# Performance work log

Hardware: AMD Instinct MI355X
Metric: run time of the kernel (lower is better)

The kernel has to match this reference:

```python
import jax, jax.numpy as jnp
import numpy as np

B, T, C = 32, 4096, 128  # batch, TRAIN_LEN, channels (= nb_filters)
K, D = 3, 8              # kernel_size, dilation_rate
F = 128                  # nb_filters


def my_deconv1d(x, kernel, bias, dilation):
    """Faithful MyDeConv1D: dilated transposed conv via scatter-add.

    Original: raw[b,t,k,f] = sum_c(x[b,t,c]*W[c,k,f] + bias[f])
              => einsum + C_in*bias (bias added before the C-sum!).
    Then each raw[b,t,j,:] contributes to output position t + j*d,
    summed over t (gather_nd + double reduce_sum), keep last T steps.
    """
    b, t_len, c_in = x.shape
    _, k_size, f_out = kernel.shape
    raw = jnp.einsum('btc,ckf->btkf', x, kernel) + c_in * bias  # (B,T,K,F)
    final_len = t_len + (k_size - 1) * dilation
    pos = (jnp.arange(t_len)[:, None] + jnp.arange(k_size)[None, :] * dilation).reshape(-1)  # (T*K,)
    out = jnp.zeros((b, final_len, f_out), x.dtype)
    out = out.at[:, pos, :].add(raw.reshape(b, t_len * k_size, f_out))
    return out[:, -t_len:, :]


def setup_inputs() -> dict:
    key = jax.random.key(0)
    k1, k2, k3, k4, k5 = jax.random.split(key, 5)
    he = lambda k, shape, fan_in: jax.random.normal(k, shape, jnp.float32) * np.sqrt(2.0 / fan_in)
    return {
        'x': jax.random.normal(k1, (B, T, C), jnp.float32),
        'kernel1': he(k2, (C, K, F), C * K),
        'bias1': jnp.zeros((F,), jnp.float32),
        'kernel2': he(k3, (F, K, F), F * K),
        'bias2': jnp.zeros((F,), jnp.float32),
    }


def reference(x, kernel1, bias1, kernel2, bias2):
    # TemporalDeConvBlock: repeat_times=2, residual=True, norm_way=None,
    # dropout_rate=0 (identity), activation='relu', identity shape-match.
    h = jax.nn.relu(my_deconv1d(x, kernel1, bias1, D))
    h = jax.nn.relu(my_deconv1d(h, kernel2, bias2, D))
    return jax.nn.relu(h + x)
```

## Files before the change

### kernel.cpp

```cpp
#include <hip/hip_runtime.h>
#include <hip/hip_fp16.h>

#define BATCH 32
#define TLEN  4096
#define CH    128
#define KW    3
#define DIL   8

#define BM    128
#define HR    (BM + 2 * DIL)
#define WROWS (BM + 4 * DIL)
#define LDSC  132

typedef _Float16 f16x8 __attribute__((ext_vector_type(8)));
typedef float    f32x4 __attribute__((ext_vector_type(4)));

__global__ void prep_weights_kernel(const float* __restrict__ W1,
                                    const float* __restrict__ W2,
                                    _Float16* __restrict__ Wt1,
                                    _Float16* __restrict__ Wt2) {
    const int total = KW * CH * CH;
    int idx = blockIdx.x * 256 + threadIdx.x;
    if (idx >= 2 * total) return;
    const float* W  = (idx < total) ? W1 : W2;
    _Float16*    Wt = (idx < total) ? Wt1 : Wt2;
    int r = idx % total;
    int j = r / (CH * CH);
    int f = (r / CH) % CH;
    int c = r % CH;
    Wt[j * CH * CH + f * CH + c] = (_Float16)W[c * (KW * CH) + j * CH + f];
}

__global__ __launch_bounds__(256)
void fused_deconv_kernel(const float* __restrict__ x,
                         const _Float16* __restrict__ Wt1,
                         const float* __restrict__ bias1,
                         const _Float16* __restrict__ Wt2,
                         const float* __restrict__ bias2,
                         float* __restrict__ out)
{
    __shared__ __align__(16) _Float16 xs[WROWS][LDSC];
    __shared__ __align__(16) _Float16 hs[HR][LDSC];

    const int tid  = threadIdx.x;
    const int lane = tid & 63;
    const int wid  = tid >> 6;
    const int l15  = lane & 15;
    const int kg   = lane >> 4;
    const int nc   = wid << 5;

    const int bt0 = blockIdx.x;
    const int bt  = (bt0 & 7) * 128 + (bt0 >> 3);

    const int b  = bt >> 5;
    const int t0 = (bt & 31) << 7;

    f16x8 w1[12][2];
#pragma unroll
    for (int ks = 0; ks < 12; ++ks) {
        const int j  = ks >> 2;
        const int c0 = (ks & 3) << 5;
        const _Float16* wb = Wt1 + (size_t)j * (CH * CH) + c0 + kg * 8;
        w1[ks][0] = *(const f16x8*)(wb + (nc + l15) * CH);
        w1[ks][1] = *(const f16x8*)(wb + (nc + 16 + l15) * CH);
    }

#pragma unroll
    for (int p = 0; p < 10; ++p) {
        const int i   = tid + 256 * p;
        const int row = i >> 4;
        const int c8  = (i & 15) << 3;
        const int t   = t0 + row;
        f16x8 o;
        if (t < TLEN) {
            const float* xp = x + ((size_t)b * TLEN + t) * CH + c8;
            f32x4 v0 = *(const f32x4*)(xp + 0);
            f32x4 v1 = *(const f32x4*)(xp + 4);
            o[0] = (_Float16)v0[0]; o[1] = (_Float16)v0[1];
            o[2] = (_Float16)v0[2]; o[3] = (_Float16)v0[3];
            o[4] = (_Float16)v1[0]; o[5] = (_Float16)v1[1];
            o[6] = (_Float16)v1[2]; o[7] = (_Float16)v1[3];
        } else {
            o = (f16x8){};
        }
        *(f16x8*)&xs[row][c8] = o;
    }

    const float bv1_0 = 128.0f * bias1[nc + l15];
    const float bv1_1 = 128.0f * bias1[nc + 16 + l15];
    const float bv2_0 = 128.0f * bias2[nc + l15];
    const float bv2_1 = 128.0f * bias2[nc + 16 + l15];

    __syncthreads();

    f32x4 acc1[9][2];
#pragma unroll
    for (int m = 0; m < 9; ++m) {
        acc1[m][0] = (f32x4){0.f, 0.f, 0.f, 0.f};
        acc1[m][1] = (f32x4){0.f, 0.f, 0.f, 0.f};
    }
#pragma unroll
    for (int ks = 0; ks < 12; ++ks) {
        const int j     = ks >> 2;
        const int c0    = (ks & 3) << 5;
        const int shift = (2 - j) * DIL;
#pragma unroll
        for (int m = 0; m < 9; ++m) {
            f16x8 af = *(const f16x8*)&xs[m * 16 + shift + l15][c0 + kg * 8];
            acc1[m][0] = __builtin_amdgcn_mfma_f32_16x16x32_f16(af, w1[ks][0], acc1[m][0], 0, 0, 0);
            acc1[m][1] = __builtin_amdgcn_mfma_f32_16x16x32_f16(af, w1[ks][1], acc1[m][1], 0, 0, 0);
        }
    }

    f16x8 w2[12][2];
#pragma unroll
    for (int ks = 0; ks < 12; ++ks) {
        const int j  = ks >> 2;
        const int c0 = (ks & 3) << 5;
        const _Float16* wb = Wt2 + (size_t)j * (CH * CH) + c0 + kg * 8;
        w2[ks][0] = *(const f16x8*)(wb + (nc + l15) * CH);
        w2[ks][1] = *(const f16x8*)(wb + (nc + 16 + l15) * CH);
    }

#pragma unroll
    for (int m = 0; m < 9; ++m) {
#pragma unroll
        for (int nn = 0; nn < 2; ++nn) {
            const float bv = nn ? bv1_1 : bv1_0;
            const int f = nc + nn * 16 + l15;
#pragma unroll
            for (int i = 0; i < 4; ++i) {
                const int r = m * 16 + kg * 4 + i;
                const int u = t0 + r;
                const int nv = 1 + (u < TLEN - DIL) + (u < TLEN - 2 * DIL);
                float v = acc1[m][nn][i] + (float)nv * bv;
                v = fmaxf(v, 0.0f);
                hs[r][f] = (u < TLEN) ? (_Float16)v : (_Float16)0.0f;
            }
        }
    }
    __syncthreads();

    f32x4 acc2[8][2];
#pragma unroll
    for (int m = 0; m < 8; ++m) {
        acc2[m][0] = (f32x4){0.f, 0.f, 0.f, 0.f};
        acc2[m][1] = (f32x4){0.f, 0.f, 0.f, 0.f};
    }
#pragma unroll
    for (int ks = 0; ks < 12; ++ks) {
        const int j     = ks >> 2;
        const int c0    = (ks & 3) << 5;
        const int shift = (2 - j) * DIL;
#pragma unroll
        for (int m = 0; m < 8; ++m) {
            f16x8 af = *(const f16x8*)&hs[m * 16 + shift + l15][c0 + kg * 8];
            acc2[m][0] = __builtin_amdgcn_mfma_f32_16x16x32_f16(af, w2[ks][0], acc2[m][0], 0, 0, 0);
            acc2[m][1] = __builtin_amdgcn_mfma_f32_16x16x32_f16(af, w2[ks][1], acc2[m][1], 0, 0, 0);
        }
    }

#pragma unroll
    for (int m = 0; m < 8; ++m) {
#pragma unroll
        for (int nn = 0; nn < 2; ++nn) {
            const float bv = nn ? bv2_1 : bv2_0;
            const int f = nc + nn * 16 + l15;
#pragma unroll
            for (int i = 0; i < 4; ++i) {
                const int r = m * 16 + kg * 4 + i;
                const int t = t0 + r;
                const int nv = 1 + (t < TLEN - DIL) + (t < TLEN - 2 * DIL);
                float v = acc2[m][nn][i] + (float)nv * bv;
                v = fmaxf(v, 0.0f);
                v = fmaxf(v + (float)xs[r][f], 0.0f);
                out[((size_t)b * TLEN + t) * CH + f] = v;
            }
        }
    }
}

extern "C" void kernel_launch(void* const* d_in, const int* in_sizes, int n_in,
                              void* d_out, int out_size, void* d_ws, size_t ws_size,
                              hipStream_t stream) {
    const float* x  = (const float*)d_in[0];
    const float* W1 = (const float*)d_in[1];
    const float* b1 = (const float*)d_in[2];
    const float* W2 = (const float*)d_in[3];
    const float* b2 = (const float*)d_in[4];
    float* out = (float*)d_out;

    _Float16* Wt1 = (_Float16*)d_ws;
    _Float16* Wt2 = Wt1 + KW * CH * CH;

    prep_weights_kernel<<<(2 * KW * CH * CH + 255) / 256, 256, 0, stream>>>(W1, W2, Wt1, Wt2);

    const int grid = BATCH * (TLEN / BM);
    fused_deconv_kernel<<<grid, 256, 0, stream>>>(x, Wt1, b1, Wt2, b2, out);
}
```

Baseline: 66.62 us.

## Precast x to fp16 and load tiles via async global-to-LDS with XOR swizzle

Adds a separate pass converting x to fp16 in workspace, then the fused kernel loads tiles directly into LDS with global_load_lds. LDS padding is replaced by an XOR swizzle layout to avoid bank conflicts. The aim is to cut register staging and conversion in the main kernel. It costs an extra full read and write of x and an extra launch, raising total memory traffic.

```diff
diff --git a/kernel.cpp b/kernel.cpp
--- a/kernel.cpp
+++ b/kernel.cpp
@@ -10,10 +10,11 @@
 #define BM    128
 #define HR    (BM + 2 * DIL)
 #define WROWS (BM + 4 * DIL)
-#define LDSC  132
 
 typedef _Float16 f16x8 __attribute__((ext_vector_type(8)));
 typedef float    f32x4 __attribute__((ext_vector_type(4)));
+
+#define SWZ(row, e) ((row) * CH + ((e) ^ (((row) & 7) << 3)))
 
 __global__ void prep_weights_kernel(const float* __restrict__ W1,
                                     const float* __restrict__ W2,
@@ -32,21 +33,40 @@
 }
 
 __global__ __launch_bounds__(256)
-void fused_deconv_kernel(const float* __restrict__ x,
+void x_to_f16_kernel(const float* __restrict__ x, _Float16* __restrict__ xh) {
+    const size_t stride = (size_t)2048 * 256;
+    const size_t i0 = (size_t)blockIdx.x * 256 + threadIdx.x;
+#pragma unroll
+    for (int k = 0; k < 4; ++k) {
+        const size_t idx = (i0 + (size_t)k * stride) * 8;
+        f32x4 v0 = *(const f32x4*)(x + idx);
+        f32x4 v1 = *(const f32x4*)(x + idx + 4);
+        f16x8 o;
+        o[0] = (_Float16)v0[0]; o[1] = (_Float16)v0[1];
+        o[2] = (_Float16)v0[2]; o[3] = (_Float16)v0[3];
+        o[4] = (_Float16)v1[0]; o[5] = (_Float16)v1[1];
+        o[6] = (_Float16)v1[2]; o[7] = (_Float16)v1[3];
+        *(f16x8*)&xh[idx] = o;
+    }
+}
+
+__global__ __launch_bounds__(256)
+void fused_deconv_kernel(const _Float16* __restrict__ xh,
                          const _Float16* __restrict__ Wt1,
                          const float* __restrict__ bias1,
                          const _Float16* __restrict__ Wt2,
                          const float* __restrict__ bias2,
                          float* __restrict__ out)
 {
-    __shared__ __align__(16) _Float16 xs[WROWS][LDSC];
-    __shared__ __align__(16) _Float16 hs[HR][LDSC];
+    __shared__ __align__(16) _Float16 xs[WROWS * CH];
+    __shared__ __align__(16) _Float16 hs[HR * CH];
 
     const int tid  = threadIdx.x;
     const int lane = tid & 63;
     const int wid  = tid >> 6;
     const int l15  = lane & 15;
     const int kg   = lane >> 4;
+    const int kg8  = kg << 3;
     const int nc   = wid << 5;
 
     const int bt0 = blockIdx.x;
@@ -60,30 +80,30 @@
     for (int ks = 0; ks < 12; ++ks) {
         const int j  = ks >> 2;
         const int c0 = (ks & 3) << 5;
-        const _Float16* wb = Wt1 + (size_t)j * (CH * CH) + c0 + kg * 8;
+        const _Float16* wb = Wt1 + (size_t)j * (CH * CH) + c0 + kg8;
         w1[ks][0] = *(const f16x8*)(wb + (nc + l15) * CH);
         w1[ks][1] = *(const f16x8*)(wb + (nc + 16 + l15) * CH);
     }
 
-#pragma unroll
-    for (int p = 0; p < 10; ++p) {
-        const int i   = tid + 256 * p;
-        const int row = i >> 4;
-        const int c8  = (i & 15) << 3;
-        const int t   = t0 + row;
-        f16x8 o;
-        if (t < TLEN) {
-            const float* xp = x + ((size_t)b * TLEN + t) * CH + c8;
-            f32x4 v0 = *(const f32x4*)(xp + 0);
-            f32x4 v1 = *(const f32x4*)(xp + 4);
-            o[0] = (_Float16)v0[0]; o[1] = (_Float16)v0[1];
-            o[2] = (_Float16)v0[2]; o[3] = (_Float16)v0[3];
-            o[4] = (_Float16)v1[0]; o[5] = (_Float16)v1[1];
-            o[6] = (_Float16)v1[2]; o[7] = (_Float16)v1[3];
-        } else {
-            o = (f16x8){};
-        }
-        *(f16x8*)&xs[row][c8] = o;
+    {
+        const int rbase = wid * 40;
+#pragma unroll
+        for (int k = 0; k < 10; ++k) {
+            const int r0  = rbase + k * 4;
+            _Float16* dst = &xs[r0 * CH];
+            const int row = r0 + (lane >> 4);
+            if (t0 + r0 + 3 < TLEN) {
+                const _Float16* src = xh + ((size_t)b * TLEN + (t0 + row)) * CH
+                                      + ((l15 ^ (row & 7)) << 3);
+                __builtin_amdgcn_global_load_lds(
+                    (const __attribute__((address_space(1))) void*)src,
+                    (__attribute__((address_space(3))) void*)dst,
+                    16, 0, 0);
+            } else {
+                f16x8 z = {};
+                *(f16x8*)(dst + lane * 8) = z;
+            }
+        }
     }
 
     const float bv1_0 = 128.0f * bias1[nc + l15];
@@ -106,7 +126,8 @@
         const int shift = (2 - j) * DIL;
 #pragma unroll
         for (int m = 0; m < 9; ++m) {
-            f16x8 af = *(const f16x8*)&xs[m * 16 + shift + l15][c0 + kg * 8];
+            const int row = m * 16 + shift + l15;
+            f16x8 af = *(const f16x8*)&xs[SWZ(row, c0 + kg8)];
             acc1[m][0] = __builtin_amdgcn_mfma_f32_16x16x32_f16(af, w1[ks][0], acc1[m][0], 0, 0, 0);
             acc1[m][1] = __builtin_amdgcn_mfma_f32_16x16x32_f16(af, w1[ks][1], acc1[m][1], 0, 0, 0);
         }
@@ -117,7 +138,7 @@
     for (int ks = 0; ks < 12; ++ks) {
         const int j  = ks >> 2;
         const int c0 = (ks & 3) << 5;
-        const _Float16* wb = Wt2 + (size_t)j * (CH * CH) + c0 + kg * 8;
+        const _Float16* wb = Wt2 + (size_t)j * (CH * CH) + c0 + kg8;
         w2[ks][0] = *(const f16x8*)(wb + (nc + l15) * CH);
         w2[ks][1] = *(const f16x8*)(wb + (nc + 16 + l15) * CH);
     }
@@ -135,7 +156,7 @@
                 const int nv = 1 + (u < TLEN - DIL) + (u < TLEN - 2 * DIL);
                 float v = acc1[m][nn][i] + (float)nv * bv;
                 v = fmaxf(v, 0.0f);
-                hs[r][f] = (u < TLEN) ? (_Float16)v : (_Float16)0.0f;
+                hs[SWZ(r, f)] = (u < TLEN) ? (_Float16)v : (_Float16)0.0f;
             }
         }
     }
@@ -154,7 +175,8 @@
         const int shift = (2 - j) * DIL;
 #pragma unroll
         for (int m = 0; m < 8; ++m) {
-            f16x8 af = *(const f16x8*)&hs[m * 16 + shift + l15][c0 + kg * 8];
+            const int row = m * 16 + shift + l15;
+            f16x8 af = *(const f16x8*)&hs[SWZ(row, c0 + kg8)];
             acc2[m][0] = __builtin_amdgcn_mfma_f32_16x16x32_f16(af, w2[ks][0], acc2[m][0], 0, 0, 0);
             acc2[m][1] = __builtin_amdgcn_mfma_f32_16x16x32_f16(af, w2[ks][1], acc2[m][1], 0, 0, 0);
         }
@@ -173,7 +195,7 @@
                 const int nv = 1 + (t < TLEN - DIL) + (t < TLEN - 2 * DIL);
                 float v = acc2[m][nn][i] + (float)nv * bv;
                 v = fmaxf(v, 0.0f);
-                v = fmaxf(v + (float)xs[r][f], 0.0f);
+                v = fmaxf(v + (float)xs[SWZ(r, f)], 0.0f);
                 out[((size_t)b * TLEN + t) * CH + f] = v;
             }
         }
@@ -190,11 +212,13 @@
     const float* b2 = (const float*)d_in[4];
     float* out = (float*)d_out;
 
-    _Float16* Wt1 = (_Float16*)d_ws;
+    _Float16* xh  = (_Float16*)d_ws;
+    _Float16* Wt1 = xh + (size_t)BATCH * TLEN * CH;
     _Float16* Wt2 = Wt1 + KW * CH * CH;
 
     prep_weights_kernel<<<(2 * KW * CH * CH + 255) / 256, 256, 0, stream>>>(W1, W2, Wt1, Wt2);
+    x_to_f16_kernel<<<2048, 256, 0, stream>>>(x, xh);
 
     const int grid = BATCH * (TLEN / BM);
-    fused_deconv_kernel<<<grid, 256, 0, stream>>>(x, Wt1, b1, Wt2, b2, out);
-}
+    fused_deconv_kernel<<<grid, 256, 0, stream>>>(xh, Wt1, b1, Wt2, b2, out);
+}
```

After: 86.28 us. 1.3x slower.
